# Kernel tuning notes

Measured on AMD Instinct MI355X. Metric: run time of the kernel, lower is better.

The kernel has to match this reference:

```python
import jax, jax.numpy as jnp
import numpy as np

C = 1.5          # Poincare ball curvature (geoopt PoincareBallExact(c=1.5))
TEMP = 0.1       # logits temperature
EPS = 1e-5       # artanh clamp, matches geoopt fp32 eps


def _mlp(x, w1, b1, w2, b2, w3, b3):
    # torch nn.GELU default is the exact erf formulation
    h = jax.nn.gelu(x @ w1 + b1, approximate=False)
    h = jax.nn.gelu(h @ w2 + b2, approximate=False)
    return h @ w3 + b3


def _expmap0(u):
    # geoopt expmap0: tanh(sqrt(c)*||u||) * u / (sqrt(c)*||u||)
    sqrt_c = jnp.sqrt(C)
    n = jnp.maximum(jnp.linalg.norm(u, axis=-1, keepdims=True), 1e-15)
    return jnp.tanh(sqrt_c * n) * u / (sqrt_c * n)


def _poincare_dist(protos, y):
    """Pairwise Poincare distance. protos: (P, d) on-ball, y: (B, d) on-ball -> (B, P).
    dist(x, y) = 2/sqrt(c) * artanh(sqrt(c) * ||mobius_add(-x, y)||)
    """
    sqrt_c = jnp.sqrt(C)
    x = -protos                               # (P, d)
    x2 = jnp.sum(x * x, axis=-1)              # (P,)
    y2 = jnp.sum(y * y, axis=-1)              # (B,)
    xy = y @ x.T                              # (B, P) = <x, y> broadcast
    a = 1.0 + 2.0 * C * xy + C * y2[:, None]  # coeff of x
    b = 1.0 - C * x2[None, :]                 # coeff of y
    denom = 1.0 + 2.0 * C * xy + (C * C) * x2[None, :] * y2[:, None]
    denom = jnp.maximum(jnp.abs(denom), 1e-15)
    # only one (B, P, d) intermediate: the mobius-add numerator
    num = a[:, :, None] * x[None, :, :] + b[:, :, None] * y[:, None, :]
    r = sqrt_c * jnp.linalg.norm(num, axis=-1) / denom   # (B, P)
    r = jnp.clip(r, 0.0, 1.0 - EPS)
    return (2.0 / sqrt_c) * jnp.arctanh(r)


def setup_inputs() -> dict:
    key = jax.random.key(0)
    ks = jax.random.split(key, 16)
    B, DIN, H, D = 64, 768, 4096, 256
    PG, PS = 500, 5000

    def lin(kw, kb, fan_in, fan_out):
        s = 1.0 / np.sqrt(fan_in)
        w = jax.random.uniform(kw, (fan_in, fan_out), jnp.float32, -s, s)
        b = jax.random.uniform(kb, (fan_out,), jnp.float32, -s, s)
        return w, b

    x = jax.random.normal(ks[0], (B, DIN), jnp.float32)
    # prototypes: random points well inside the ball (radius 1/sqrt(1.5) ~ 0.816)
    protos_genus = 0.01 * jax.random.normal(ks[1], (PG, D), jnp.float32)
    protos_species = 0.01 * jax.random.normal(ks[2], (PS, D), jnp.float32)

    w1g, b1g = lin(ks[3], ks[4], DIN, H)
    w2g, b2g = lin(ks[5], ks[6], H, H)
    w3g, b3g = lin(ks[7], ks[8], H, D)
    w1s, b1s = lin(ks[9], ks[10], DIN, H)
    w2s, b2s = lin(ks[11], ks[12], H, H)
    w3s, b3s = lin(ks[13], ks[14], H, D)

    return {
        "x": x, "protos_genus": protos_genus, "protos_species": protos_species,
        "w1g": w1g, "b1g": b1g, "w2g": w2g, "b2g": b2g, "w3g": w3g, "b3g": b3g,
        "w1s": w1s, "b1s": b1s, "w2s": w2s, "b2s": b2s, "w3s": w3s, "b3s": b3s,
    }


def reference(x, protos_genus, protos_species,
              w1g, b1g, w2g, b2g, w3g, b3g,
              w1s, b1s, w2s, b2s, w3s, b3s):
    feat_g = _mlp(x, w1g, b1g, w2g, b2g, w3g, b3g)   # (B, D) euclidean
    feat_s = _mlp(x, w1s, b1s, w2s, b2s, w3s, b3s)
    hyp_g = _expmap0(feat_g)
    hyp_s = _expmap0(feat_s)
    logits_g = -_poincare_dist(protos_genus, hyp_g) / TEMP    # (B, PG)
    logits_s = -_poincare_dist(protos_species, hyp_s) / TEMP  # (B, PS)
    return (logits_g, logits_s)
```

## Files before the change

### kernel.cpp

```cpp
#include <hip/hip_runtime.h>
#include <hip/hip_bf16.h>
#include <math.h>

typedef unsigned short ushort_t;
typedef unsigned int uint_t;

#define C_CURV 1.5f
#define SQRT_C 1.22474487139158905f
#define TEMP_ 0.1f

typedef __attribute__((ext_vector_type(8))) short short8;
typedef __attribute__((ext_vector_type(4))) float f32x4;

static __device__ __forceinline__ ushort_t f2bf(float f) {
  union { float f; uint_t u; } v; v.f = f;
  uint_t u = v.u;
  uint_t r = (u + 0x7FFFu + ((u >> 16) & 1u)) >> 16;
  return (ushort_t)r;
}

static __device__ __forceinline__ float b2f(ushort_t h) {
  union { uint_t u; float f; } v; v.u = ((uint_t)h) << 16;
  return v.f;
}

static __device__ __forceinline__ float gelu_exact(float x) {
  return 0.5f * x * (1.0f + erff(x * 0.70710678118654752f));
}

#define GLOAD_LDS16(gp, lp) __builtin_amdgcn_global_load_lds( \
    (const __attribute__((address_space(1))) void*)(const void*)(gp), \
    (__attribute__((address_space(3))) void*)(void*)(lp), 16, 0, 0)

__global__ void k_cvt_x(const float* __restrict__ x, ushort_t* __restrict__ xb, int n4) {
  int i = blockIdx.x * blockDim.x + threadIdx.x;
  if (i >= n4) return;
  float4 v = reinterpret_cast<const float4*>(x)[i];
  ushort4 o;
  o.x = f2bf(v.x); o.y = f2bf(v.y); o.z = f2bf(v.z); o.w = f2bf(v.w);
  reinterpret_cast<ushort4*>(xb)[i] = o;
}

__global__ __launch_bounds__(512, 4) void k_gemm(
    const ushort_t* __restrict__ Abase, long a_br_stride,
    const float* __restrict__ Wg, const float* __restrict__ Ws,
    ushort_t* __restrict__ partial, int N, int K, int kchunk)
{
  __shared__ float    sW[3][32][128];
  __shared__ ushort_t sA[3][64][32];

  const int tn = blockIdx.x, ks = blockIdx.y, br = blockIdx.z;
  const int KS = gridDim.y;
  const ushort_t* A = Abase + (long)br * a_br_stride;
  const float* W = br ? Ws : Wg;
  const int lane = threadIdx.x & 63;
  const int w = threadIdx.x >> 6;
  const int c = lane & 15;
  const int g = lane >> 4;
  const int n0b = tn * 128;
  const int k0 = ks * kchunk;
  const bool hasA = (w < 4);

  const float* wst = W + (long)(k0 + w * 4 + (lane >> 5)) * N + n0b + (lane & 31) * 4;
  const ushort_t* ast = A + (long)(w * 16 + (lane >> 2)) * K + k0 + (lane & 3) * 8;

  f32x4 acc[4];
  #pragma unroll
  for (int mi = 0; mi < 4; ++mi) acc[mi] = f32x4{0.f, 0.f, 0.f, 0.f};

#define STAGE(buf, t) do { \
    GLOAD_LDS16(wst + (long)((t) * 32) * N,     &sW[buf][w * 4][0]); \
    GLOAD_LDS16(wst + (long)((t) * 32 + 2) * N, &sW[buf][w * 4 + 2][0]); \
    if (hasA) GLOAD_LDS16(ast + (t) * 32, &sA[buf][w * 16][0]); \
  } while (0)

#define COMPUTE(buf) do { \
    short8 af[4]; \
    _Pragma("unroll") for (int mi = 0; mi < 4; ++mi) \
      af[mi] = *reinterpret_cast<const short8*>(&sA[buf][c + 16 * mi][8 * g]); \
    float bw[8]; \
    _Pragma("unroll") for (int j = 0; j < 8; ++j) \
      bw[j] = sW[buf][8 * g + j][w * 16 + c]; \
    short8 bf; \
    _Pragma("unroll") for (int j = 0; j < 8; ++j) bf[j] = (short)f2bf(bw[j]); \
    _Pragma("unroll") for (int mi = 0; mi < 4; ++mi) \
      acc[mi] = __builtin_amdgcn_mfma_f32_16x16x32_bf16(af[mi], bf, acc[mi], 0, 0, 0); \
  } while (0)

  const int nt = kchunk >> 5;
  STAGE(0, 0);
  STAGE(1, 1);
  int t = 0;
  for (; t < nt - 1; ++t) {
    if (hasA) asm volatile("s_waitcnt vmcnt(3)" ::: "memory");
    else      asm volatile("s_waitcnt vmcnt(2)" ::: "memory");
    __builtin_amdgcn_s_barrier();
    if (t + 2 < nt) STAGE((t + 2) % 3, t + 2);
    COMPUTE(t % 3);
  }
  asm volatile("s_waitcnt vmcnt(0)" ::: "memory");
  __builtin_amdgcn_s_barrier();
  COMPUTE(t % 3);
#undef STAGE
#undef COMPUTE

  ushort_t* po = partial + (long)(br * KS + ks) * 64 * N;
  const int n0 = n0b + w * 16 + c;
  #pragma unroll
  for (int mi = 0; mi < 4; ++mi)
    #pragma unroll
    for (int q = 0; q < 4; ++q) {
      int b = 16 * mi + 4 * g + q;
      po[(long)b * N + n0] = f2bf(acc[mi][q]);
    }
}

__global__ void k_reduce_gelu(const ushort_t* __restrict__ partial,
    const float* __restrict__ bg, const float* __restrict__ bs,
    ushort_t* __restrict__ hb, int N, int KS, int total8)
{
  int i = blockIdx.x * blockDim.x + threadIdx.x;
  if (i >= total8) return;
  int perbr8 = 64 * N / 8;
  int br = i / perbr8;
  int rem = i - br * perbr8;
  const short8* pp = reinterpret_cast<const short8*>(partial) + (long)br * KS * perbr8 + rem;
  float s[8] = {0.f, 0.f, 0.f, 0.f, 0.f, 0.f, 0.f, 0.f};
  for (int ks = 0; ks < KS; ++ks) {
    short8 t = pp[(long)ks * perbr8];
    #pragma unroll
    for (int j = 0; j < 8; ++j) s[j] += b2f((ushort_t)t[j]);
  }
  int n8 = rem % (N / 8);
  float4 bv0 = reinterpret_cast<const float4*>(br ? bs : bg)[n8 * 2];
  float4 bv1 = reinterpret_cast<const float4*>(br ? bs : bg)[n8 * 2 + 1];
  s[0] += bv0.x; s[1] += bv0.y; s[2] += bv0.z; s[3] += bv0.w;
  s[4] += bv1.x; s[5] += bv1.y; s[6] += bv1.z; s[7] += bv1.w;
  short8 o;
  #pragma unroll
  for (int j = 0; j < 8; ++j) o[j] = (short)f2bf(gelu_exact(s[j]));
  reinterpret_cast<short8*>(hb)[i] = o;
}

__global__ __launch_bounds__(256) void k_expmap(const ushort_t* __restrict__ partial,
    const float* __restrict__ b3g, const float* __restrict__ b3s,
    ushort_t* __restrict__ hypb, float* __restrict__ y2, int KS)
{
  int b = blockIdx.x, br = blockIdx.y, d = threadIdx.x;
  const ushort_t* pp = partial + (long)(br * KS) * 64 * 256 + (long)b * 256 + d;
  float s = 0.f;
  #pragma unroll 8
  for (int ks = 0; ks < KS; ++ks) s += b2f(pp[(long)ks * 64 * 256]);
  s += (br ? b3s : b3g)[d];

  float v = s * s;
  #pragma unroll
  for (int off = 1; off < 64; off <<= 1) v += __shfl_xor(v, off);
  __shared__ float red[4];
  __shared__ float n2s;
  if ((threadIdx.x & 63) == 0) red[threadIdx.x >> 6] = v;
  __syncthreads();
  if (threadIdx.x == 0) n2s = red[0] + red[1] + red[2] + red[3];
  __syncthreads();
  float n = fmaxf(sqrtf(n2s), 1e-15f);
  float sn = SQRT_C * n;
  float t = tanhf(sn);
  float scale = t / sn;
  hypb[((long)br * 64 + b) * 256 + d] = f2bf(s * scale);
  if (threadIdx.x == 0) y2[br * 64 + b] = t * t / C_CURV;
}

__global__ __launch_bounds__(256) void k_dist(const float* __restrict__ pg,
    const float* __restrict__ ps, const ushort_t* __restrict__ hypb,
    const float* __restrict__ y2, float* __restrict__ out)
{
  int u = blockIdx.x * 4 + (threadIdx.x >> 6);
  const int lane = threadIdx.x & 63;
  const int c = lane & 15, g = lane >> 4;
  const float* protos; const ushort_t* A; const float* y2p; float* ob; int P;
  if (u < 128) {
    protos = pg; P = 500; A = hypb; y2p = y2; ob = out;
  } else {
    u -= 128;
    if (u >= 1252) return;
    protos = ps; P = 5000; A = hypb + 64 * 256; y2p = y2 + 64; ob = out + 64 * 500;
  }
  const int w = u >> 2;
  const int mi = u & 3;
  int p = w * 16 + c;
  int pc = min(p, P - 1);
  const float* pp = protos + (long)pc * 256 + 8 * g;
  const ushort_t* ap = A + (long)(c + 16 * mi) * 256 + 8 * g;

  f32x4 acc = {0.f, 0.f, 0.f, 0.f};
  float x2p = 0.f;

  #pragma unroll
  for (int s8 = 0; s8 < 8; ++s8) {
    float4 v0 = *reinterpret_cast<const float4*>(pp + 32 * s8);
    float4 v1 = *reinterpret_cast<const float4*>(pp + 32 * s8 + 4);
    x2p += v0.x * v0.x + v0.y * v0.y + v0.z * v0.z + v0.w * v0.w
         + v1.x * v1.x + v1.y * v1.y + v1.z * v1.z + v1.w * v1.w;
    short8 bfr;
    bfr[0] = (short)f2bf(v0.x); bfr[1] = (short)f2bf(v0.y);
    bfr[2] = (short)f2bf(v0.z); bfr[3] = (short)f2bf(v0.w);
    bfr[4] = (short)f2bf(v1.x); bfr[5] = (short)f2bf(v1.y);
    bfr[6] = (short)f2bf(v1.z); bfr[7] = (short)f2bf(v1.w);
    short8 af = *reinterpret_cast<const short8*>(ap + 32 * s8);
    acc = __builtin_amdgcn_mfma_f32_16x16x32_bf16(af, bfr, acc, 0, 0, 0);
  }
  x2p += __shfl_xor(x2p, 16);
  x2p += __shfl_xor(x2p, 32);
  const float x2 = x2p;
  const float bb = 1.f - C_CURV * x2;
  const float LC = -2.f / (SQRT_C * TEMP_);

  if (p < P) {
    #pragma unroll
    for (int q = 0; q < 4; ++q) {
      int b = 16 * mi + 4 * g + q;
      float xy = -acc[q];
      float y2v = y2p[b];
      float a = 1.f + 2.f * C_CURV * xy + C_CURV * y2v;
      float den = fabsf(1.f + 2.f * C_CURV * xy + C_CURV * C_CURV * x2 * y2v);
      den = fmaxf(den, 1e-15f);
      float num2 = a * a * x2 + 2.f * a * bb * xy + bb * bb * y2v;
      num2 = fmaxf(num2, 0.f);
      float r = SQRT_C * sqrtf(num2) / den;
      r = fminf(r, 1.f - 1e-5f);
      r = fmaxf(r, 0.f);
      ob[(long)b * P + p] = LC * atanhf(r);
    }
  }
}

extern "C" void kernel_launch(void* const* d_in, const int* in_sizes, int n_in,
                              void* d_out, int out_size, void* d_ws, size_t ws_size,
                              hipStream_t stream) {
  const float* x   = (const float*)d_in[0];
  const float* pg  = (const float*)d_in[1];
  const float* ps  = (const float*)d_in[2];
  const float* w1g = (const float*)d_in[3];
  const float* b1g = (const float*)d_in[4];
  const float* w2g = (const float*)d_in[5];
  const float* b2g = (const float*)d_in[6];
  const float* w3g = (const float*)d_in[7];
  const float* b3g = (const float*)d_in[8];
  const float* w1s = (const float*)d_in[9];
  const float* b1s = (const float*)d_in[10];
  const float* w2s = (const float*)d_in[11];
  const float* b2s = (const float*)d_in[12];
  const float* w3s = (const float*)d_in[13];
  const float* b3s = (const float*)d_in[14];
  float* out = (float*)d_out;
  char* ws = (char*)d_ws;
  (void)in_sizes; (void)n_in; (void)out_size; (void)ws_size;

  const int KS1 = 8, KS2 = 8, KS3 = 32;
  size_t PART = (size_t)KS2 * 2 * 64 * 4096 * 2;

  ushort_t* partial = (ushort_t*)(ws);
  ushort_t* xb      = (ushort_t*)(ws + PART);
  ushort_t* h1b     = (ushort_t*)(ws + PART + 98304);
  ushort_t* h2b     = (ushort_t*)(ws + PART + 98304 + 1048576);
  ushort_t* hypb    = (ushort_t*)(ws + PART + 98304 + 2097152);
  float*    y2      = (float*)   (ws + PART + 98304 + 2097152 + 65536);

  k_cvt_x<<<48, 256, 0, stream>>>(x, xb, 64 * 768 / 4);
  k_gemm<<<dim3(32, KS1, 2), 512, 0, stream>>>(xb, 0L, w1g, w1s, partial, 4096, 768, 768 / KS1);
  k_reduce_gelu<<<256, 256, 0, stream>>>(partial, b1g, b1s, h1b, 4096, KS1, 2 * 64 * 4096 / 8);
  k_gemm<<<dim3(32, KS2, 2), 512, 0, stream>>>(h1b, (long)64 * 4096, w2g, w2s, partial, 4096, 4096, 4096 / KS2);
  k_reduce_gelu<<<256, 256, 0, stream>>>(partial, b2g, b2s, h2b, 4096, KS2, 2 * 64 * 4096 / 8);
  k_gemm<<<dim3(2, KS3, 2), 512, 0, stream>>>(h2b, (long)64 * 4096, w3g, w3s, partial, 256, 4096, 4096 / KS3);
  k_expmap<<<dim3(64, 2), 256, 0, stream>>>(partial, b3g, b3s, hypb, y2, KS3);
  k_dist<<<345, 256, 0, stream>>>(pg, ps, hypb, y2, out);
}
```

Before: 71.62 us.

## Stage GEMM tiles through registers with double-buffered LDS and raise split-K

The GEMM kernel no longer uses direct global-to-LDS async loads with a triple buffer. It now loads the next K tile into registers while the current tile is written to a double-buffered LDS and then computed, separated by explicit waits and scheduling barriers. The split-K factor goes from 8 to 16 for the second layer and from 32 to 64 for the third, giving more blocks to cover the streaming of fp32 weights. The cost is larger bf16 partial buffers to write and reduce, and the loads are exposed for longer since only one tile is in flight.

New measurement: 78.01 us. 8.9% more time.

```diff
diff --git a/kernel.cpp b/kernel.cpp
--- a/kernel.cpp
+++ b/kernel.cpp
@@ -27,10 +27,6 @@
 static __device__ __forceinline__ float gelu_exact(float x) {
   return 0.5f * x * (1.0f + erff(x * 0.70710678118654752f));
 }
-
-#define GLOAD_LDS16(gp, lp) __builtin_amdgcn_global_load_lds( \
-    (const __attribute__((address_space(1))) void*)(const void*)(gp), \
-    (__attribute__((address_space(3))) void*)(void*)(lp), 16, 0, 0)
 
 __global__ void k_cvt_x(const float* __restrict__ x, ushort_t* __restrict__ xb, int n4) {
   int i = blockIdx.x * blockDim.x + threadIdx.x;
@@ -46,8 +42,8 @@
     const float* __restrict__ Wg, const float* __restrict__ Ws,
     ushort_t* __restrict__ partial, int N, int K, int kchunk)
 {
-  __shared__ float    sW[3][32][128];
-  __shared__ ushort_t sA[3][64][32];
+  __shared__ float    sW[2][32][128];
+  __shared__ ushort_t sA[2][64][32];
 
   const int tn = blockIdx.x, ks = blockIdx.y, br = blockIdx.z;
   const int KS = gridDim.y;
@@ -68,41 +64,57 @@
   #pragma unroll
   for (int mi = 0; mi < 4; ++mi) acc[mi] = f32x4{0.f, 0.f, 0.f, 0.f};
 
-#define STAGE(buf, t) do { \
-    GLOAD_LDS16(wst + (long)((t) * 32) * N,     &sW[buf][w * 4][0]); \
-    GLOAD_LDS16(wst + (long)((t) * 32 + 2) * N, &sW[buf][w * 4 + 2][0]); \
-    if (hasA) GLOAD_LDS16(ast + (t) * 32, &sA[buf][w * 16][0]); \
-  } while (0)
-
-#define COMPUTE(buf) do { \
+  float4 w0A, w1A; uint4 aA;
+  float4 w0B, w1B; uint4 aB;
+
+#define LOADREG(S, T) do { \
+    w0##S = *reinterpret_cast<const float4*>(wst + (long)((T) * 32) * N); \
+    w1##S = *reinterpret_cast<const float4*>(wst + (long)((T) * 32 + 2) * N); \
+    if (hasA) a##S = *reinterpret_cast<const uint4*>(ast + (T) * 32); \
+  } while (0)
+
+#define DSWRITE(S, B) do { \
+    *reinterpret_cast<float4*>(&sW[B][w * 4 + (lane >> 5)][(lane & 31) * 4]) = w0##S; \
+    *reinterpret_cast<float4*>(&sW[B][w * 4 + 2 + (lane >> 5)][(lane & 31) * 4]) = w1##S; \
+    if (hasA) *reinterpret_cast<uint4*>(&sA[B][w * 16 + (lane >> 2)][(lane & 3) * 8]) = a##S; \
+  } while (0)
+
+#define COMPUTE(B) do { \
     short8 af[4]; \
     _Pragma("unroll") for (int mi = 0; mi < 4; ++mi) \
-      af[mi] = *reinterpret_cast<const short8*>(&sA[buf][c + 16 * mi][8 * g]); \
+      af[mi] = *reinterpret_cast<const short8*>(&sA[B][c + 16 * mi][8 * g]); \
     float bw[8]; \
     _Pragma("unroll") for (int j = 0; j < 8; ++j) \
-      bw[j] = sW[buf][8 * g + j][w * 16 + c]; \
+      bw[j] = sW[B][8 * g + j][w * 16 + c]; \
     short8 bf; \
     _Pragma("unroll") for (int j = 0; j < 8; ++j) bf[j] = (short)f2bf(bw[j]); \
     _Pragma("unroll") for (int mi = 0; mi < 4; ++mi) \
       acc[mi] = __builtin_amdgcn_mfma_f32_16x16x32_bf16(af[mi], bf, acc[mi], 0, 0, 0); \
   } while (0)
 
+#define ITER(CUR, NXT, T) do { \
+    if ((T) + 1 < nt) LOADREG(NXT, (T) + 1); \
+    __builtin_amdgcn_sched_barrier(0); \
+    DSWRITE(CUR, (T) & 1); \
+    asm volatile("s_waitcnt lgkmcnt(0)" ::: "memory"); \
+    __builtin_amdgcn_sched_barrier(0); \
+    __builtin_amdgcn_s_barrier(); \
+    __builtin_amdgcn_sched_barrier(0); \
+    COMPUTE((T) & 1); \
+  } while (0)
+
   const int nt = kchunk >> 5;
-  STAGE(0, 0);
-  STAGE(1, 1);
+  LOADREG(A, 0);
   int t = 0;
-  for (; t < nt - 1; ++t) {
-    if (hasA) asm volatile("s_waitcnt vmcnt(3)" ::: "memory");
-    else      asm volatile("s_waitcnt vmcnt(2)" ::: "memory");
-    __builtin_amdgcn_s_barrier();
-    if (t + 2 < nt) STAGE((t + 2) % 3, t + 2);
-    COMPUTE(t % 3);
-  }
-  asm volatile("s_waitcnt vmcnt(0)" ::: "memory");
-  __builtin_amdgcn_s_barrier();
-  COMPUTE(t % 3);
-#undef STAGE
+  for (; t + 1 < nt; t += 2) {
+    ITER(A, B, t);
+    ITER(B, A, t + 1);
+  }
+  if (nt & 1) ITER(A, B, nt - 1);
+#undef LOADREG
+#undef DSWRITE
 #undef COMPUTE
+#undef ITER
 
   ushort_t* po = partial + (long)(br * KS + ks) * 64 * N;
   const int n0 = n0b + w * 16 + c;
@@ -256,7 +268,7 @@
   char* ws = (char*)d_ws;
   (void)in_sizes; (void)n_in; (void)out_size; (void)ws_size;
 
-  const int KS1 = 8, KS2 = 8, KS3 = 32;
+  const int KS1 = 8, KS2 = 16, KS3 = 64;
   size_t PART = (size_t)KS2 * 2 * 64 * 4096 * 2;
 
   ushort_t* partial = (ushort_t*)(ws);
```
